# Optimization experiments

Measured on AMD Instinct MI355X. Metric: run time of the kernel, lower is better.

The kernel has to match this reference:

```python
import jax, jax.numpy as jnp
import numpy as np

N = 500_000          # number of tree nodes
K = 8                # attributes per group
ROWS, COLS = 2048, 4096   # image size; P = ROWS*COLS pixels


def _build_euler_tour(n, seed=0):
    """Random tree (parent[i] < i, parent[0] = 0) + real DFS Euler tour with a
    single timer incremented on both entry (tpre) and exit (tpost)."""
    rng = np.random.default_rng(seed)
    parent = np.zeros(n, dtype=np.int64)
    if n > 1:
        parent[1:] = np.floor(rng.random(n - 1) * np.arange(1, n)).astype(np.int64)
    counts = np.bincount(parent[1:], minlength=n)
    starts = np.zeros(n, dtype=np.int64)
    starts[1:] = np.cumsum(counts)[:-1]
    child_order = np.argsort(parent[1:], kind='stable') + 1  # children grouped by parent
    tpre = np.empty(n, dtype=np.int64)
    tpost = np.empty(n, dtype=np.int64)
    next_child = starts.copy()
    ends = starts + counts
    stack = np.empty(n, dtype=np.int64)
    sp = 0
    stack[0] = 0
    timer = 0
    tpre[0] = timer; timer += 1
    while sp >= 0:
        u = stack[sp]
        if next_child[u] < ends[u]:
            v = child_order[next_child[u]]
            next_child[u] += 1
            sp += 1
            stack[sp] = v
            tpre[v] = timer; timer += 1
        else:
            tpost[u] = timer; timer += 1
            sp -= 1
    return tpre, tpost


def setup_inputs() -> dict:
    key = jax.random.key(0)
    k1, k2, k3, k4 = jax.random.split(key, 4)
    tpre_np, tpost_np = _build_euler_tour(N)
    weight = jax.random.normal(k1, (K,), dtype=jnp.float32) * 0.1
    bias = jnp.zeros((1,), dtype=jnp.float32)
    residues = jax.random.normal(k2, (N,), dtype=jnp.float32)
    attrs2d = jax.random.uniform(k3, (N, K), dtype=jnp.float32)
    node_of_pixel = jax.random.randint(k4, (ROWS * COLS,), 0, N)
    return {
        'weight': weight,
        'bias': bias,
        'residues': residues,
        'attrs2d': attrs2d,
        'tpre': jnp.asarray(tpre_np),
        'tpost': jnp.asarray(tpost_np),
        'node_of_pixel': node_of_pixel,
        'numRows': ROWS,
        'numCols': COLS,
    }


def reference(weight, bias, residues, attrs2d, tpre, tpost, node_of_pixel, numRows, numCols):
    beta_f = 1.0  # module default; clamp_logits=False
    # logits = attrs2d @ w + b ; filtered residues per node
    logits = attrs2d @ weight + bias[0]                     # (N,)
    sig = jax.nn.sigmoid(beta_f * logits)                   # (N,)
    filtered = residues * sig                                # (N,)
    # implicit J.T @ filtered via Euler-tour scatter + prefix scan
    T = 2 * tpre.shape[0]                                    # tpost.max()+1 for a full DFS tour
    delta = (jnp.zeros((T,), dtype=filtered.dtype)
             .at[tpre].add(filtered)
             .at[tpost].add(-filtered))
    y_cumsum = jnp.cumsum(delta)                             # (2N,)
    y = y_cumsum[tpre[node_of_pixel]]                        # (P,) gather per pixel
    return y.reshape(numRows, numCols)
```

## Files before the change

### kernel.cpp

```cpp
#include <hip/hip_runtime.h>

#define SCAN_THREADS 256
#define EPT 8
#define CHUNK (SCAN_THREADS * EPT)
#define CHUNK_SHIFT 11
#define MAX_CHUNKS 1024

typedef int   v2i __attribute__((ext_vector_type(2)));
typedef int   v4i __attribute__((ext_vector_type(4)));
typedef float v2f __attribute__((ext_vector_type(2)));
typedef float v4f __attribute__((ext_vector_type(4)));

__global__ void k1_filter_scatter_hist(const float* __restrict__ attrs,
                                       const float* __restrict__ weight,
                                       const float* __restrict__ bias,
                                       const float* __restrict__ residues,
                                       const int* __restrict__ tpre,
                                       const int* __restrict__ tpost,
                                       float* __restrict__ delta,
                                       float* __restrict__ partials,
                                       int N, int numChunks) {
    __shared__ float hist[MAX_CHUNKS];
    for (int i = threadIdx.x; i < numChunks; i += SCAN_THREADS) hist[i] = 0.0f;
    __syncthreads();

    int u0 = (blockIdx.x * blockDim.x + threadIdx.x) * 2;
    v4f w0 = *(const v4f*)weight;
    v4f w1 = *(const v4f*)(weight + 4);
    float b = bias[0];
    if (u0 + 2 <= N) {
        v2f rr = __builtin_nontemporal_load((const v2f*)(residues + u0));
        v2i pr = __builtin_nontemporal_load((const v2i*)(tpre + u0));
        v2i po = __builtin_nontemporal_load((const v2i*)(tpost + u0));
        v4f a00 = __builtin_nontemporal_load((const v4f*)(attrs + (size_t)u0 * 8));
        v4f a01 = __builtin_nontemporal_load((const v4f*)(attrs + (size_t)u0 * 8 + 4));
        v4f a10 = __builtin_nontemporal_load((const v4f*)(attrs + (size_t)u0 * 8 + 8));
        v4f a11 = __builtin_nontemporal_load((const v4f*)(attrs + (size_t)u0 * 8 + 12));
        float l0 = a00.x*w0.x + a00.y*w0.y + a00.z*w0.z + a00.w*w0.w +
                   a01.x*w1.x + a01.y*w1.y + a01.z*w1.z + a01.w*w1.w + b;
        float l1 = a10.x*w0.x + a10.y*w0.y + a10.z*w0.z + a10.w*w0.w +
                   a11.x*w1.x + a11.y*w1.y + a11.z*w1.z + a11.w*w1.w + b;
        float f0 = rr.x / (1.0f + __expf(-l0));
        float f1 = rr.y / (1.0f + __expf(-l1));
        delta[pr.x] =  f0; delta[pr.y] =  f1;
        delta[po.x] = -f0; delta[po.y] = -f1;
        atomicAdd(&hist[pr.x >> CHUNK_SHIFT],  f0);
        atomicAdd(&hist[pr.y >> CHUNK_SHIFT],  f1);
        atomicAdd(&hist[po.x >> CHUNK_SHIFT], -f0);
        atomicAdd(&hist[po.y >> CHUNK_SHIFT], -f1);
    } else {
        for (int u = u0; u < N; ++u) {
            float logit = b;
            #pragma unroll
            for (int k = 0; k < 8; ++k) logit += attrs[(size_t)u * 8 + k] * weight[k];
            float f = residues[u] / (1.0f + __expf(-logit));
            int pre = tpre[u], pos = tpost[u];
            delta[pre] =  f;
            delta[pos] = -f;
            atomicAdd(&hist[pre >> CHUNK_SHIFT],  f);
            atomicAdd(&hist[pos >> CHUNK_SHIFT], -f);
        }
    }
    __syncthreads();
    for (int i = threadIdx.x; i < numChunks; i += SCAN_THREADS)
        atomicAdd(&partials[i], hist[i]);
}

__global__ void k1_filter_scatter(const float* __restrict__ attrs,
                                  const float* __restrict__ weight,
                                  const float* __restrict__ bias,
                                  const float* __restrict__ residues,
                                  const int* __restrict__ tpre,
                                  const int* __restrict__ tpost,
                                  float* __restrict__ delta,
                                  int N) {
    int u0 = (blockIdx.x * blockDim.x + threadIdx.x) * 2;
    v4f w0 = *(const v4f*)weight;
    v4f w1 = *(const v4f*)(weight + 4);
    float b = bias[0];
    if (u0 + 2 <= N) {
        v2f rr = *(const v2f*)(residues + u0);
        v2i pr = *(const v2i*)(tpre + u0);
        v2i po = *(const v2i*)(tpost + u0);
        v4f a00 = *(const v4f*)(attrs + (size_t)u0 * 8);
        v4f a01 = *(const v4f*)(attrs + (size_t)u0 * 8 + 4);
        v4f a10 = *(const v4f*)(attrs + (size_t)u0 * 8 + 8);
        v4f a11 = *(const v4f*)(attrs + (size_t)u0 * 8 + 12);
        float l0 = a00.x*w0.x + a00.y*w0.y + a00.z*w0.z + a00.w*w0.w +
                   a01.x*w1.x + a01.y*w1.y + a01.z*w1.z + a01.w*w1.w + b;
        float l1 = a10.x*w0.x + a10.y*w0.y + a10.z*w0.z + a10.w*w0.w +
                   a11.x*w1.x + a11.y*w1.y + a11.z*w1.z + a11.w*w1.w + b;
        float f0 = rr.x / (1.0f + __expf(-l0));
        float f1 = rr.y / (1.0f + __expf(-l1));
        delta[pr.x] =  f0; delta[pr.y] =  f1;
        delta[po.x] = -f0; delta[po.y] = -f1;
    } else {
        for (int u = u0; u < N; ++u) {
            float logit = b;
            #pragma unroll
            for (int k = 0; k < 8; ++k) logit += attrs[(size_t)u * 8 + k] * weight[k];
            float f = residues[u] / (1.0f + __expf(-logit));
            delta[tpre[u]]  =  f;
            delta[tpost[u]] = -f;
        }
    }
}

__global__ void k2_partials(const float* __restrict__ delta,
                            float* __restrict__ partials, int T) {
    __shared__ float sdata[SCAN_THREADS / 64];
    int base = blockIdx.x * CHUNK + threadIdx.x * EPT;
    float s = 0.0f;
    if (base + EPT <= T) {
        v4f v0 = *(const v4f*)(delta + base);
        v4f v1 = *(const v4f*)(delta + base + 4);
        s = v0.x + v0.y + v0.z + v0.w + v1.x + v1.y + v1.z + v1.w;
    } else {
        for (int i = 0; i < EPT; ++i)
            if (base + i < T) s += delta[base + i];
    }
    #pragma unroll
    for (int d = 32; d > 0; d >>= 1) s += __shfl_down(s, d, 64);
    int lane = threadIdx.x & 63, wid = threadIdx.x >> 6;
    if (lane == 0) sdata[wid] = s;
    __syncthreads();
    if (threadIdx.x == 0)
        partials[blockIdx.x] = sdata[0] + sdata[1] + sdata[2] + sdata[3];
}

__global__ void k4_scan_chunks(float* __restrict__ data,
                               const float* __restrict__ partials, int T) {
    __shared__ float wavesums[SCAN_THREADS / 64];
    __shared__ float redsum[SCAN_THREADS / 64];
    int lane = threadIdx.x & 63, wid = threadIdx.x >> 6;

    float c = 0.0f;
    for (int i = threadIdx.x; i < blockIdx.x; i += SCAN_THREADS)
        c += partials[i];
    #pragma unroll
    for (int d = 32; d > 0; d >>= 1) c += __shfl_down(c, d, 64);
    if (lane == 0) redsum[wid] = c;

    int base = blockIdx.x * CHUNK + threadIdx.x * EPT;
    float v[EPT];
    bool full = (base + EPT <= T);
    if (full) {
        v4f v0 = *(const v4f*)(data + base);
        v4f v1 = *(const v4f*)(data + base + 4);
        v[0]=v0.x; v[1]=v0.y; v[2]=v0.z; v[3]=v0.w;
        v[4]=v1.x; v[5]=v1.y; v[6]=v1.z; v[7]=v1.w;
    } else {
        for (int i = 0; i < EPT; ++i)
            v[i] = (base + i < T) ? data[base + i] : 0.0f;
    }
    float run = 0.0f;
    #pragma unroll
    for (int i = 0; i < EPT; ++i) { run += v[i]; v[i] = run; }
    float tot = run;
    float x = tot;
    #pragma unroll
    for (int d = 1; d < 64; d <<= 1) {
        float y = __shfl_up(x, d, 64);
        if (lane >= d) x += y;
    }
    if (lane == 63) wavesums[wid] = x;
    __syncthreads();
    float woff = 0.0f, offset = redsum[0] + redsum[1] + redsum[2] + redsum[3];
    #pragma unroll
    for (int i = 0; i < SCAN_THREADS / 64; ++i)
        if (i < wid) woff += wavesums[i];
    float add = (x - tot) + woff + offset;
    if (full) {
        v4f o0 = { v[0]+add, v[1]+add, v[2]+add, v[3]+add };
        v4f o1 = { v[4]+add, v[5]+add, v[6]+add, v[7]+add };
        *(v4f*)(data + base)     = o0;
        *(v4f*)(data + base + 4) = o1;
    } else {
        for (int i = 0; i < EPT; ++i)
            if (base + i < T) data[base + i] = v[i] + add;
    }
}

__global__ void k5_node_values(const float* __restrict__ ycum,
                               const int* __restrict__ tpre,
                               float* __restrict__ vnode, int N) {
    int u0 = (blockIdx.x * blockDim.x + threadIdx.x) * 4;
    if (u0 + 4 <= N) {
        v4i t = __builtin_nontemporal_load((const v4i*)(tpre + u0));
        v4f y = { ycum[t.x], ycum[t.y], ycum[t.z], ycum[t.w] };
        *(v4f*)(vnode + u0) = y;
    } else {
        for (int u = u0; u < N; ++u) vnode[u] = ycum[tpre[u]];
    }
}

__global__ void k6_gather(const float* __restrict__ vnode,
                          const int* __restrict__ nop,
                          float* __restrict__ out, int P) {
    int i = (blockIdx.x * blockDim.x + threadIdx.x) * 8;
    if (i + 8 <= P) {
        v4i n0 = __builtin_nontemporal_load((const v4i*)(nop + i));
        v4i n1 = __builtin_nontemporal_load((const v4i*)(nop + i + 4));
        v4f o0 = { vnode[n0.x], vnode[n0.y], vnode[n0.z], vnode[n0.w] };
        v4f o1 = { vnode[n1.x], vnode[n1.y], vnode[n1.z], vnode[n1.w] };
        __builtin_nontemporal_store(o0, (v4f*)(out + i));
        __builtin_nontemporal_store(o1, (v4f*)(out + i + 4));
    } else {
        for (; i < P; ++i) out[i] = vnode[nop[i]];
    }
}

__global__ void k6_direct(const float* __restrict__ ycum,
                          const int* __restrict__ tpre,
                          const int* __restrict__ nop,
                          float* __restrict__ out, int P) {
    int i = (blockIdx.x * blockDim.x + threadIdx.x) * 4;
    if (i + 4 <= P) {
        v4i n = *(const v4i*)(nop + i);
        v4f o = { ycum[tpre[n.x]], ycum[tpre[n.y]], ycum[tpre[n.z]], ycum[tpre[n.w]] };
        *(v4f*)(out + i) = o;
    } else {
        for (; i < P; ++i) out[i] = ycum[tpre[nop[i]]];
    }
}

extern "C" void kernel_launch(void* const* d_in, const int* in_sizes, int n_in,
                              void* d_out, int out_size, void* d_ws, size_t ws_size,
                              hipStream_t stream) {
    const float* weight   = (const float*)d_in[0];
    const float* bias     = (const float*)d_in[1];
    const float* residues = (const float*)d_in[2];
    const float* attrs    = (const float*)d_in[3];
    const int*   tpre     = (const int*)d_in[4];
    const int*   tpost    = (const int*)d_in[5];
    const int*   nop      = (const int*)d_in[6];
    float* out = (float*)d_out;

    const int N = in_sizes[2];
    const int T = 2 * N;
    const int P = out_size;
    const int numChunks = (T + CHUNK - 1) / CHUNK;

    size_t needFull = (size_t)(T + N + 1024) * sizeof(float);
    size_t needMid  = (size_t)(N + 1024) * sizeof(float);

    float* delta;
    float* vnode    = nullptr;
    float* partials;
    bool useVnode = true;

    if (ws_size >= needFull) {
        delta    = (float*)d_ws;
        vnode    = delta + T;
        partials = vnode + N;
    } else if (ws_size >= needMid) {
        delta    = out;
        vnode    = (float*)d_ws;
        partials = vnode + N;
    } else {
        delta    = out;
        partials = (float*)d_ws;
        useVnode = false;
    }

    const int k1Blocks = (N / 2 + 255) / 256;

    if (numChunks <= MAX_CHUNKS) {
        (void)hipMemsetAsync(partials, 0, (size_t)numChunks * sizeof(float), stream);
        k1_filter_scatter_hist<<<k1Blocks, 256, 0, stream>>>(
            attrs, weight, bias, residues, tpre, tpost, delta, partials, N, numChunks);
    } else {
        k1_filter_scatter<<<k1Blocks, 256, 0, stream>>>(
            attrs, weight, bias, residues, tpre, tpost, delta, N);
        k2_partials<<<numChunks, SCAN_THREADS, 0, stream>>>(delta, partials, T);
    }

    k4_scan_chunks<<<numChunks, SCAN_THREADS, 0, stream>>>(delta, partials, T);

    if (useVnode) {
        k5_node_values<<<(N / 4 + 255) / 256, 256, 0, stream>>>(delta, tpre, vnode, N);
        int gatherBlocks = (P / 8 + 255) / 256;
        k6_gather<<<gatherBlocks, 256, 0, stream>>>(vnode, nop, out, P);
    } else {
        int gatherBlocks = (P / 4 + 255) / 256;
        k6_direct<<<gatherBlocks, 256, 0, stream>>>(delta, tpre, nop, out, P);
    }
}
```

Measured before the change: 188.3 us.

## Replace histogram-partials scan with single-pass decoupled lookback scan

Drops the shared-memory chunk histogram and its atomics from the filter/scatter kernel, along with the memset. The prefix scan becomes one kernel that passes chunk totals between blocks through a packed flag/value lookback array, with a warp-wide lookback and spin-wait. The gather kernel's output stores change from nontemporal to regular stores. The lookback depends on earlier blocks making forward progress, and the spin-waits can add latency if blocks are scheduled out of order.

After: 197.6 us. 1.05x slower.

```diff
diff --git a/kernel.cpp b/kernel.cpp
--- a/kernel.cpp
+++ b/kernel.cpp
@@ -3,7 +3,6 @@
 #define SCAN_THREADS 256
 #define EPT 8
 #define CHUNK (SCAN_THREADS * EPT)
-#define CHUNK_SHIFT 11
 #define MAX_CHUNKS 1024
 
 typedef int   v2i __attribute__((ext_vector_type(2)));
@@ -11,19 +10,23 @@
 typedef float v2f __attribute__((ext_vector_type(2)));
 typedef float v4f __attribute__((ext_vector_type(4)));
 
-__global__ void k1_filter_scatter_hist(const float* __restrict__ attrs,
-                                       const float* __restrict__ weight,
-                                       const float* __restrict__ bias,
-                                       const float* __restrict__ residues,
-                                       const int* __restrict__ tpre,
-                                       const int* __restrict__ tpost,
-                                       float* __restrict__ delta,
-                                       float* __restrict__ partials,
-                                       int N, int numChunks) {
-    __shared__ float hist[MAX_CHUNKS];
-    for (int i = threadIdx.x; i < numChunks; i += SCAN_THREADS) hist[i] = 0.0f;
-    __syncthreads();
-
+__device__ __forceinline__ unsigned long long lb_pack(int flag, float v) {
+    return ((unsigned long long)(unsigned)flag << 32) |
+           (unsigned long long)__float_as_uint(v);
+}
+
+__global__ void k1_filter_scatter(const float* __restrict__ attrs,
+                                  const float* __restrict__ weight,
+                                  const float* __restrict__ bias,
+                                  const float* __restrict__ residues,
+                                  const int* __restrict__ tpre,
+                                  const int* __restrict__ tpost,
+                                  float* __restrict__ delta,
+                                  unsigned long long* lb,
+                                  int N, int numChunks) {
+    if (lb && blockIdx.x == 0) {
+        for (int i = threadIdx.x; i < numChunks; i += blockDim.x) lb[i] = 0ull;
+    }
     int u0 = (blockIdx.x * blockDim.x + threadIdx.x) * 2;
     v4f w0 = *(const v4f*)weight;
     v4f w1 = *(const v4f*)(weight + 4);
@@ -44,56 +47,6 @@
         float f1 = rr.y / (1.0f + __expf(-l1));
         delta[pr.x] =  f0; delta[pr.y] =  f1;
         delta[po.x] = -f0; delta[po.y] = -f1;
-        atomicAdd(&hist[pr.x >> CHUNK_SHIFT],  f0);
-        atomicAdd(&hist[pr.y >> CHUNK_SHIFT],  f1);
-        atomicAdd(&hist[po.x >> CHUNK_SHIFT], -f0);
-        atomicAdd(&hist[po.y >> CHUNK_SHIFT], -f1);
-    } else {
-        for (int u = u0; u < N; ++u) {
-            float logit = b;
-            #pragma unroll
-            for (int k = 0; k < 8; ++k) logit += attrs[(size_t)u * 8 + k] * weight[k];
-            float f = residues[u] / (1.0f + __expf(-logit));
-            int pre = tpre[u], pos = tpost[u];
-            delta[pre] =  f;
-            delta[pos] = -f;
-            atomicAdd(&hist[pre >> CHUNK_SHIFT],  f);
-            atomicAdd(&hist[pos >> CHUNK_SHIFT], -f);
-        }
-    }
-    __syncthreads();
-    for (int i = threadIdx.x; i < numChunks; i += SCAN_THREADS)
-        atomicAdd(&partials[i], hist[i]);
-}
-
-__global__ void k1_filter_scatter(const float* __restrict__ attrs,
-                                  const float* __restrict__ weight,
-                                  const float* __restrict__ bias,
-                                  const float* __restrict__ residues,
-                                  const int* __restrict__ tpre,
-                                  const int* __restrict__ tpost,
-                                  float* __restrict__ delta,
-                                  int N) {
-    int u0 = (blockIdx.x * blockDim.x + threadIdx.x) * 2;
-    v4f w0 = *(const v4f*)weight;
-    v4f w1 = *(const v4f*)(weight + 4);
-    float b = bias[0];
-    if (u0 + 2 <= N) {
-        v2f rr = *(const v2f*)(residues + u0);
-        v2i pr = *(const v2i*)(tpre + u0);
-        v2i po = *(const v2i*)(tpost + u0);
-        v4f a00 = *(const v4f*)(attrs + (size_t)u0 * 8);
-        v4f a01 = *(const v4f*)(attrs + (size_t)u0 * 8 + 4);
-        v4f a10 = *(const v4f*)(attrs + (size_t)u0 * 8 + 8);
-        v4f a11 = *(const v4f*)(attrs + (size_t)u0 * 8 + 12);
-        float l0 = a00.x*w0.x + a00.y*w0.y + a00.z*w0.z + a00.w*w0.w +
-                   a01.x*w1.x + a01.y*w1.y + a01.z*w1.z + a01.w*w1.w + b;
-        float l1 = a10.x*w0.x + a10.y*w0.y + a10.z*w0.z + a10.w*w0.w +
-                   a11.x*w1.x + a11.y*w1.y + a11.z*w1.z + a11.w*w1.w + b;
-        float f0 = rr.x / (1.0f + __expf(-l0));
-        float f1 = rr.y / (1.0f + __expf(-l1));
-        delta[pr.x] =  f0; delta[pr.y] =  f1;
-        delta[po.x] = -f0; delta[po.y] = -f1;
     } else {
         for (int u = u0; u < N; ++u) {
             float logit = b;
@@ -103,6 +56,107 @@
             delta[tpre[u]]  =  f;
             delta[tpost[u]] = -f;
         }
+    }
+}
+
+__global__ __launch_bounds__(SCAN_THREADS)
+void k_scan_lookback(float* __restrict__ data,
+                     unsigned long long* __restrict__ lb, int T) {
+    __shared__ float wavesums[SCAN_THREADS / 64];
+    __shared__ float s_excl;
+    const int c = blockIdx.x;
+    const int tid = threadIdx.x, lane = tid & 63, wid = tid >> 6;
+
+    int base = c * CHUNK + tid * EPT;
+    float v[EPT];
+    bool full = (base + EPT <= T);
+    if (full) {
+        v4f v0 = *(const v4f*)(data + base);
+        v4f v1 = *(const v4f*)(data + base + 4);
+        v[0]=v0.x; v[1]=v0.y; v[2]=v0.z; v[3]=v0.w;
+        v[4]=v1.x; v[5]=v1.y; v[6]=v1.z; v[7]=v1.w;
+    } else {
+        for (int i = 0; i < EPT; ++i)
+            v[i] = (base + i < T) ? data[base + i] : 0.0f;
+    }
+    float run = 0.0f;
+    #pragma unroll
+    for (int i = 0; i < EPT; ++i) { run += v[i]; v[i] = run; }
+    float tot = run;
+    float x = tot;
+    #pragma unroll
+    for (int d = 1; d < 64; d <<= 1) {
+        float y = __shfl_up(x, d, 64);
+        if (lane >= d) x += y;
+    }
+    if (lane == 63) wavesums[wid] = x;
+    __syncthreads();
+    float blockAgg = wavesums[0] + wavesums[1] + wavesums[2] + wavesums[3];
+
+    if (tid == 0) {
+        __hip_atomic_store(&lb[c], lb_pack(c == 0 ? 2 : 1, blockAgg),
+                           __ATOMIC_RELEASE, __HIP_MEMORY_SCOPE_AGENT);
+        if (c == 0) s_excl = 0.0f;
+    }
+
+    if (c > 0 && wid == 0) {
+        float running = 0.0f;
+        int pos = c - 1;
+        while (true) {
+            int idx = pos - lane;
+            int flag; float val;
+            if (idx >= 0) {
+                unsigned long long w = __hip_atomic_load(
+                    &lb[idx], __ATOMIC_ACQUIRE, __HIP_MEMORY_SCOPE_AGENT);
+                flag = (int)(w >> 32);
+                val  = __uint_as_float((unsigned)w);
+            } else { flag = 2; val = 0.0f; }
+            unsigned long long inclmask = __ballot(flag == 2);
+            unsigned long long invmask  = __ballot(flag == 0);
+            if (inclmask != 0) {
+                int lstar = __ffsll((long long)inclmask) - 1;
+                unsigned long long below =
+                    (lstar >= 63) ? 0x7FFFFFFFFFFFFFFFull : ((1ull << lstar) - 1ull);
+                if ((invmask & below) == 0) {
+                    float contrib = (lane <= lstar) ? val : 0.0f;
+                    #pragma unroll
+                    for (int d = 32; d > 0; d >>= 1)
+                        contrib += __shfl_down(contrib, d, 64);
+                    running += __shfl(contrib, 0, 64);
+                    break;
+                }
+            } else if (invmask == 0) {
+                float contrib = val;
+                #pragma unroll
+                for (int d = 32; d > 0; d >>= 1)
+                    contrib += __shfl_down(contrib, d, 64);
+                running += __shfl(contrib, 0, 64);
+                pos -= 64;
+                continue;
+            }
+            __builtin_amdgcn_s_sleep(1);
+        }
+        if (lane == 0) {
+            s_excl = running;
+            __hip_atomic_store(&lb[c], lb_pack(2, running + blockAgg),
+                               __ATOMIC_RELEASE, __HIP_MEMORY_SCOPE_AGENT);
+        }
+    }
+    __syncthreads();
+
+    float woff = 0.0f;
+    #pragma unroll
+    for (int i = 0; i < SCAN_THREADS / 64; ++i)
+        if (i < wid) woff += wavesums[i];
+    float add = (x - tot) + woff + s_excl;
+    if (full) {
+        v4f o0 = { v[0]+add, v[1]+add, v[2]+add, v[3]+add };
+        v4f o1 = { v[4]+add, v[5]+add, v[6]+add, v[7]+add };
+        *(v4f*)(data + base)     = o0;
+        *(v4f*)(data + base + 4) = o1;
+    } else {
+        for (int i = 0; i < EPT; ++i)
+            if (base + i < T) data[base + i] = v[i] + add;
     }
 }
 
@@ -133,7 +187,6 @@
     __shared__ float wavesums[SCAN_THREADS / 64];
     __shared__ float redsum[SCAN_THREADS / 64];
     int lane = threadIdx.x & 63, wid = threadIdx.x >> 6;
-
     float c = 0.0f;
     for (int i = threadIdx.x; i < blockIdx.x; i += SCAN_THREADS)
         c += partials[i];
@@ -203,8 +256,8 @@
         v4i n1 = __builtin_nontemporal_load((const v4i*)(nop + i + 4));
         v4f o0 = { vnode[n0.x], vnode[n0.y], vnode[n0.z], vnode[n0.w] };
         v4f o1 = { vnode[n1.x], vnode[n1.y], vnode[n1.z], vnode[n1.w] };
-        __builtin_nontemporal_store(o0, (v4f*)(out + i));
-        __builtin_nontemporal_store(o1, (v4f*)(out + i + 4));
+        *(v4f*)(out + i)     = o0;
+        *(v4f*)(out + i + 4) = o1;
     } else {
         for (; i < P; ++i) out[i] = vnode[nop[i]];
     }
@@ -241,41 +294,42 @@
     const int P = out_size;
     const int numChunks = (T + CHUNK - 1) / CHUNK;
 
-    size_t needFull = (size_t)(T + N + 1024) * sizeof(float);
-    size_t needMid  = (size_t)(N + 1024) * sizeof(float);
+    size_t needFull = (size_t)(T + N) * sizeof(float) + MAX_CHUNKS * 8 + 256;
+    size_t needMid  = (size_t)N * sizeof(float) + MAX_CHUNKS * 8 + 256;
 
     float* delta;
-    float* vnode    = nullptr;
-    float* partials;
+    float* vnode = nullptr;
+    unsigned long long* lb;
     bool useVnode = true;
 
     if (ws_size >= needFull) {
-        delta    = (float*)d_ws;
-        vnode    = delta + T;
-        partials = vnode + N;
+        delta = (float*)d_ws;
+        vnode = delta + T;
+        lb    = (unsigned long long*)(vnode + N);
     } else if (ws_size >= needMid) {
-        delta    = out;
-        vnode    = (float*)d_ws;
-        partials = vnode + N;
-    } else {
-        delta    = out;
-        partials = (float*)d_ws;
+        delta = out;
+        vnode = (float*)d_ws;
+        lb    = (unsigned long long*)(vnode + N);
+    } else {
+        delta = out;
+        lb    = (unsigned long long*)d_ws;
         useVnode = false;
     }
 
     const int k1Blocks = (N / 2 + 255) / 256;
-
-    if (numChunks <= MAX_CHUNKS) {
-        (void)hipMemsetAsync(partials, 0, (size_t)numChunks * sizeof(float), stream);
-        k1_filter_scatter_hist<<<k1Blocks, 256, 0, stream>>>(
-            attrs, weight, bias, residues, tpre, tpost, delta, partials, N, numChunks);
-    } else {
-        k1_filter_scatter<<<k1Blocks, 256, 0, stream>>>(
-            attrs, weight, bias, residues, tpre, tpost, delta, N);
+    bool lookback = (numChunks <= MAX_CHUNKS) && useVnode;
+
+    k1_filter_scatter<<<k1Blocks, 256, 0, stream>>>(
+        attrs, weight, bias, residues, tpre, tpost, delta,
+        lookback ? lb : nullptr, N, numChunks);
+
+    if (lookback) {
+        k_scan_lookback<<<numChunks, SCAN_THREADS, 0, stream>>>(delta, lb, T);
+    } else {
+        float* partials = (float*)lb;
         k2_partials<<<numChunks, SCAN_THREADS, 0, stream>>>(delta, partials, T);
-    }
-
-    k4_scan_chunks<<<numChunks, SCAN_THREADS, 0, stream>>>(delta, partials, T);
+        k4_scan_chunks<<<numChunks, SCAN_THREADS, 0, stream>>>(delta, partials, T);
+    }
 
     if (useVnode) {
         k5_node_values<<<(N / 4 + 255) / 256, 256, 0, stream>>>(delta, tpre, vnode, N);
```
